# Performance work log

Measured on AMD Instinct MI355X. Metric: run time of the kernel, lower is better.

The kernel has to match this reference:

```python
import jax, jax.numpy as jnp
import numpy as np

B, N, M, D = 64, 512, 1024, 128

def setup_inputs() -> dict:
    key = jax.random.key(0)
    ks = jax.random.split(key, 7)
    s = 1.0 / np.sqrt(D)
    return {
        "h_c": jax.random.normal(ks[0], (B, N, D), dtype=jnp.float32),
        "h_p": jax.random.normal(ks[1], (B, M, D), dtype=jnp.float32),
        "U_w": jax.random.normal(ks[2], (D, D), dtype=jnp.float32) * s,
        "U_b": jax.random.normal(ks[3], (D,), dtype=jnp.float32) * s,
        "V_w": jax.random.normal(ks[4], (D, D), dtype=jnp.float32) * s,
        "V_b": jax.random.normal(ks[5], (D,), dtype=jnp.float32) * s,
        "q": jax.random.normal(ks[6], (D,), dtype=jnp.float32),
    }

def reference(h_c, h_p, U_w, U_b, V_w, V_b, q):
    # ReLU-activated linear projections (torch Linear: x @ W.T + b)
    Uc = jax.nn.relu(jnp.einsum('bnd,ed->bne', h_c, U_w) + U_b)  # (B,N,D)
    Vp = jax.nn.relu(jnp.einsum('bmd,ed->bme', h_p, V_w) + V_b)  # (B,M,D)
    # bilinear attention scores and softmax over protein axis
    attn = jnp.einsum('bnd,bmd->bnm', Uc, Vp)                    # (B,N,M)
    weights = jax.nn.softmax(attn, axis=-1)
    context = jnp.einsum('bnm,bmd->bnd', weights, Vp)            # (B,N,D)
    joint = (Uc + context) * q                                   # (B,N,D)
    return joint.mean(axis=1)                                    # (B,D)
```

## Files before the change

### kernel.cpp

```cpp
#include <hip/hip_runtime.h>
#include <hip/hip_bf16.h>
#include <cstdint>

#define BB 64
#define NN 512
#define MM 1024
#define DD 128

typedef __bf16 bf16x8 __attribute__((ext_vector_type(8)));
typedef float f32x4 __attribute__((ext_vector_type(4)));

static __device__ __forceinline__ unsigned short f2bf(float f) {
    union { float f; unsigned int i; } v; v.f = f;
    unsigned int x = v.i;
    x += 0x7FFFu + ((x >> 16) & 1u);
    return (unsigned short)(x >> 16);
}
static __device__ __forceinline__ unsigned int f2bf2(float a, float b) {
    union { __hip_bfloat162 h; unsigned int u; } c;
    c.h = __float22bfloat162_rn(make_float2(a, b));
    return c.u;
}
static __device__ __forceinline__ void async16(const void* g, void* l) {
    __builtin_amdgcn_global_load_lds(
        (const __attribute__((address_space(1))) void*)g,
        (__attribute__((address_space(3))) void*)l, 16, 0, 0);
}

__global__ __launch_bounds__(256, 4) void proj_v_kernel(
    const float* __restrict__ X,
    const float* __restrict__ Wv,
    const float* __restrict__ bias,
    unsigned short* __restrict__ Y,
    unsigned short* __restrict__ YT)
{
    __shared__ __align__(16) unsigned short Ws[128 * 136];
    unsigned short* Ys = Ws;
    unsigned short* Ts = Ws + 8192;
    const int t = threadIdx.x;
    const int lane = t & 63;
    const int wave = t >> 6;
    const int n16 = lane & 15, q = lane >> 4;
    const long row0 = (long)blockIdx.x * 64;

    float4 xv[8];
    {
        const float* xrow = X + (row0 + wave * 16 + n16) * DD + q * 8;
        #pragma unroll
        for (int kk = 0; kk < 4; ++kk) {
            xv[2 * kk]     = *(const float4*)(xrow + kk * 32);
            xv[2 * kk + 1] = *(const float4*)(xrow + kk * 32 + 4);
        }
    }

    {
        const float4* Wg = (const float4*)Wv;
        #pragma unroll
        for (int i = 0; i < 16; ++i) {
            int idx = i * 256 + t;
            float4 v = Wg[idx];
            int off = idx * 4;
            uint2 u = { f2bf2(v.x, v.y), f2bf2(v.z, v.w) };
            *(uint2*)&Ws[(off >> 7) * 136 + (off & 127)] = u;
        }
    }
    __syncthreads();

    f32x4 acc[8];
    #pragma unroll
    for (int j = 0; j < 8; ++j) acc[j] = {0.f, 0.f, 0.f, 0.f};

    #pragma unroll
    for (int kk = 0; kk < 4; ++kk) {
        float4 x0 = xv[2 * kk], x1 = xv[2 * kk + 1];
        union { bf16x8 v; unsigned int u[4]; } a;
        a.u[0] = f2bf2(x0.x, x0.y); a.u[1] = f2bf2(x0.z, x0.w);
        a.u[2] = f2bf2(x1.x, x1.y); a.u[3] = f2bf2(x1.z, x1.w);
        #pragma unroll
        for (int j = 0; j < 8; ++j) {
            bf16x8 b = *(const bf16x8*)&Ws[(j * 16 + n16) * 136 + q * 8 + kk * 32];
            acc[j] = __builtin_amdgcn_mfma_f32_16x16x32_bf16(a.v, b, acc[j], 0, 0, 0);
        }
    }

    unsigned short yb[8][4];
    #pragma unroll
    for (int j = 0; j < 8; ++j) {
        const float bv = bias[j * 16 + n16];
        float y[4];
        #pragma unroll
        for (int r = 0; r < 4; ++r) {
            float v = acc[j][r] + bv;
            y[r] = v > 0.f ? v : 0.f;
        }
        uint2 u = { f2bf2(y[0], y[1]), f2bf2(y[2], y[3]) };
        *(uint2*)&yb[j][0] = u;
    }
    __syncthreads();

    #pragma unroll
    for (int j = 0; j < 8; ++j) {
        const int e = j * 16 + n16;
        #pragma unroll
        for (int r = 0; r < 4; ++r)
            Ys[(wave * 16 + q * 4 + r) * 128 + e] = yb[j][r];
        *(uint2*)&Ts[e * 72 + wave * 16 + q * 4] = *(uint2*)&yb[j][0];
    }
    __syncthreads();

    {
        uint4* dstY = (uint4*)(Y + row0 * DD);
        const long b = row0 >> 10;
        const long mt = (row0 & 1023) >> 6;
        uint4* dstT = (uint4*)(YT + ((b * 16 + mt) * 128) * 64);
        #pragma unroll
        for (int i = 0; i < 4; ++i) {
            int idx = i * 256 + t;
            dstY[idx] = ((const uint4*)Ys)[idx];
            int e = idx >> 3, m = (idx & 7) * 8;
            dstT[idx] = *(const uint4*)&Ts[e * 72 + m];
        }
    }
}

static __device__ __forceinline__ void bar_lgkm() {
    asm volatile("s_waitcnt lgkmcnt(0)" ::: "memory");
    __builtin_amdgcn_s_barrier();
    __builtin_amdgcn_sched_barrier(0);
}
static __device__ __forceinline__ void bar_vm8() {
    asm volatile("s_waitcnt vmcnt(8) lgkmcnt(0)" ::: "memory");
    __builtin_amdgcn_s_barrier();
    __builtin_amdgcn_sched_barrier(0);
}

static __device__ __forceinline__ void attn_iter(
    int mt, unsigned short* smem, unsigned short* Ps,
    const unsigned short* __restrict__ vpb,
    const unsigned short* __restrict__ vtb,
    int wave, int lane, int n16, int q, int a_off,
    const bf16x8 (&Bg)[4][4],
    bf16x8 (&aC)[4], bf16x8 (&aN)[4],
    f32x4 (&O)[8], float (&lpart)[4])
{
    {
        int nx = mt + 2; if (nx > 15) nx = 15;
        const unsigned short* st = vtb + nx * 8192;
        unsigned short* dst = smem + ((mt + 2) % 3) * 8192 + wave * 2048;
        #pragma unroll
        for (int i = 0; i < 4; ++i) {
            int L = wave * 256 + i * 64 + lane;
            int r = L >> 3, sc = L & 7, c = sc ^ (r & 7);
            async16(st + r * 64 + c * 8, dst + i * 512);
        }
    }
    {
        int nx = mt + 1; if (nx > 15) nx = 15;
        const unsigned short* pa = vpb + nx * 8192 + a_off;
        #pragma unroll
        for (int kk = 0; kk < 4; ++kk)
            aN[kk] = *(const bf16x8*)(pa + kk * 32);
    }

    f32x4 S[4];
    #pragma unroll
    for (int j = 0; j < 4; ++j) S[j] = {0.f, 0.f, 0.f, 0.f};
    __builtin_amdgcn_s_setprio(1);
    #pragma unroll
    for (int kk = 0; kk < 4; ++kk) {
        #pragma unroll
        for (int j = 0; j < 4; ++j)
            S[j] = __builtin_amdgcn_mfma_f32_16x16x32_bf16(aC[kk], Bg[j][kk], S[j], 0, 0, 0);
    }
    __builtin_amdgcn_s_setprio(0);

    #pragma unroll
    for (int j = 0; j < 4; ++j) {
        float p0 = __builtin_exp2f(S[j][0]);
        float p1 = __builtin_exp2f(S[j][1]);
        float p2 = __builtin_exp2f(S[j][2]);
        float p3 = __builtin_exp2f(S[j][3]);
        lpart[j] += (p0 + p1) + (p2 + p3);
        uint2 u = { f2bf2(p0, p1), f2bf2(p2, p3) };
        *(uint2*)&Ps[(j * 16 + n16) * 72 + wave * 16 + q * 4] = u;
    }
    bar_lgkm();

    const unsigned short* VTs = smem + (mt % 3) * 8192;
    __builtin_amdgcn_s_setprio(1);
    #pragma unroll
    for (int kk = 0; kk < 2; ++kk) {
        bf16x8 a = *(const bf16x8*)&Ps[(wave * 16 + n16) * 72 + kk * 32 + q * 8];
        #pragma unroll
        for (int j = 0; j < 8; ++j) {
            bf16x8 bb = *(const bf16x8*)&VTs[(j * 16 + n16) * 64 + ((kk * 4 + q) ^ (n16 & 7)) * 8];
            O[j] = __builtin_amdgcn_mfma_f32_16x16x32_bf16(a, bb, O[j], 0, 0, 0);
        }
    }
    __builtin_amdgcn_s_setprio(0);
    bar_vm8();
}

__global__ __launch_bounds__(256, 2) void attn_kernel(
    const float* __restrict__ hc,
    const float* __restrict__ Wu,
    const float* __restrict__ Ub,
    const unsigned short* __restrict__ Vp,
    const unsigned short* __restrict__ VpT,
    float* __restrict__ part)
{
    __shared__ __align__(16) unsigned short smem[29184];
    unsigned short* Ws  = smem;
    unsigned short* Ucs = smem + 17408;
    unsigned short* Ps  = smem + 24576;

    const int t = threadIdx.x;
    const int lane = t & 63;
    const int wave = t >> 6;
    const int n16 = lane & 15, q = lane >> 4;

    const int id = blockIdx.x;
    const int xcd = id & 7;
    const int slot = id >> 3;
    const int b = xcd * 8 + (slot >> 3);
    const int nt = slot & 7;

    const unsigned short* vpb = Vp + (long)b * MM * DD;
    const unsigned short* vtb = VpT + (long)b * MM * DD;

    const float LOG2E = 1.44269504088896f;

    {
        const float4* Wg = (const float4*)Wu;
        #pragma unroll
        for (int i = 0; i < 16; ++i) {
            int idx = i * 256 + t;
            float4 v = Wg[idx];
            int off = idx * 4;
            uint2 u = { f2bf2(v.x, v.y), f2bf2(v.z, v.w) };
            *(uint2*)&Ws[(off >> 7) * 136 + (off & 127)] = u;
        }
    }
    __syncthreads();

    f32x4 acc[8];
    #pragma unroll
    for (int j = 0; j < 8; ++j) acc[j] = {0.f, 0.f, 0.f, 0.f};
    {
        const float* xrow = hc + ((long)b * NN + nt * 64 + wave * 16 + n16) * DD + q * 8;
        #pragma unroll
        for (int kk = 0; kk < 4; ++kk) {
            float4 x0 = *(const float4*)(xrow + kk * 32);
            float4 x1 = *(const float4*)(xrow + kk * 32 + 4);
            union { bf16x8 v; unsigned int u[4]; } a;
            a.u[0] = f2bf2(x0.x, x0.y); a.u[1] = f2bf2(x0.z, x0.w);
            a.u[2] = f2bf2(x1.x, x1.y); a.u[3] = f2bf2(x1.z, x1.w);
            #pragma unroll
            for (int j = 0; j < 8; ++j) {
                bf16x8 bb = *(const bf16x8*)&Ws[(j * 16 + n16) * 136 + q * 8 + kk * 32];
                acc[j] = __builtin_amdgcn_mfma_f32_16x16x32_bf16(a.v, bb, acc[j], 0, 0, 0);
            }
        }
    }
    float ucred[8];
    #pragma unroll
    for (int j = 0; j < 8; ++j) {
        const float bv = Ub[j * 16 + n16];
        float s = 0.f;
        #pragma unroll
        for (int r = 0; r < 4; ++r) {
            float v = acc[j][r] + bv;
            v = v > 0.f ? v : 0.f;
            s += v;
            Ucs[(wave * 16 + q * 4 + r) * 136 + j * 16 + n16] = f2bf(v * LOG2E);
        }
        ucred[j] = s;
    }
    __syncthreads();

    bf16x8 Bg[4][4];
    #pragma unroll
    for (int j = 0; j < 4; ++j)
        #pragma unroll
        for (int kk = 0; kk < 4; ++kk)
            Bg[j][kk] = *(const bf16x8*)&Ucs[(j * 16 + n16) * 136 + q * 8 + kk * 32];

    const int a_off = (wave * 16 + n16) * 128 + q * 8;
    bf16x8 aA[4], aB[4];
    #pragma unroll
    for (int kk = 0; kk < 4; ++kk)
        aA[kk] = *(const bf16x8*)&vpb[a_off + kk * 32];
    #pragma unroll
    for (int tt = 0; tt < 2; ++tt) {
        const unsigned short* st = vtb + tt * 8192;
        unsigned short* dst = smem + tt * 8192 + wave * 2048;
        #pragma unroll
        for (int i = 0; i < 4; ++i) {
            int L = wave * 256 + i * 64 + lane;
            int r = L >> 3, sc = L & 7, c = sc ^ (r & 7);
            async16(st + r * 64 + c * 8, dst + i * 512);
        }
    }
    asm volatile("s_waitcnt vmcnt(4) lgkmcnt(0)" ::: "memory");
    __builtin_amdgcn_s_barrier();
    __builtin_amdgcn_sched_barrier(0);

    f32x4 O[8];
    #pragma unroll
    for (int j = 0; j < 8; ++j) O[j] = {0.f, 0.f, 0.f, 0.f};
    float lpart[4] = {0.f, 0.f, 0.f, 0.f};

    #pragma unroll 1
    for (int mt = 0; mt < 16; mt += 2) {
        attn_iter(mt,     smem, Ps, vpb, vtb, wave, lane, n16, q, a_off, Bg, aA, aB, O, lpart);
        attn_iter(mt + 1, smem, Ps, vpb, vtb, wave, lane, n16, q, a_off, Bg, aB, aA, O, lpart);
    }

    #pragma unroll
    for (int j = 0; j < 4; ++j) {
        lpart[j] += __shfl_xor(lpart[j], 16);
        lpart[j] += __shfl_xor(lpart[j], 32);
    }
    float* lred = (float*)Ps;
    float* red  = (float*)Ps + 256;
    if (q == 0) {
        #pragma unroll
        for (int j = 0; j < 4; ++j)
            lred[wave * 64 + j * 16 + n16] = lpart[j];
    }
    __syncthreads();

    float inv[4];
    #pragma unroll
    for (int r = 0; r < 4; ++r) {
        int n = wave * 16 + q * 4 + r;
        inv[r] = 1.0f / (lred[n] + lred[64 + n] + lred[128 + n] + lred[192 + n]);
    }

    #pragma unroll
    for (int j = 0; j < 8; ++j) {
        float s = ucred[j]
                + O[j][0] * inv[0] + O[j][1] * inv[1]
                + O[j][2] * inv[2] + O[j][3] * inv[3];
        s += __shfl_xor(s, 16);
        s += __shfl_xor(s, 32);
        if (q == 0)
            red[wave * 128 + j * 16 + n16] = s;
    }
    __syncthreads();
    if (t < 128) {
        float tot = red[t] + red[128 + t] + red[256 + t] + red[384 + t];
        part[(long)(b * 8 + nt) * DD + t] = tot;
    }
}

__global__ __launch_bounds__(256) void finalize_kernel(
    const float* __restrict__ part, const float* __restrict__ qv,
    float* __restrict__ out)
{
    int i = blockIdx.x * 256 + threadIdx.x;
    int b = i >> 7, d = i & 127;
    const float* p = part + (long)b * 8 * DD + d;
    float s = 0.f;
    #pragma unroll
    for (int nt = 0; nt < 8; ++nt) s += p[nt * DD];
    out[i] = s * qv[d] * (1.0f / (float)NN);
}

extern "C" void kernel_launch(void* const* d_in, const int* in_sizes, int n_in,
                              void* d_out, int out_size, void* d_ws, size_t ws_size,
                              hipStream_t stream) {
    const float* h_c = (const float*)d_in[0];
    const float* h_p = (const float*)d_in[1];
    const float* U_w = (const float*)d_in[2];
    const float* U_b = (const float*)d_in[3];
    const float* V_w = (const float*)d_in[4];
    const float* V_b = (const float*)d_in[5];
    const float* qv  = (const float*)d_in[6];
    float* out = (float*)d_out;

    unsigned short* Vp  = (unsigned short*)d_ws;
    unsigned short* VpT = Vp + (size_t)BB * MM * DD;
    float* part = (float*)(VpT + (size_t)BB * MM * DD);

    proj_v_kernel<<<BB * MM / 64, 256, 0, stream>>>(h_p, V_w, V_b, Vp, VpT);
    attn_kernel<<<512, 256, 0, stream>>>(h_c, U_w, U_b, Vp, VpT, part);
    finalize_kernel<<<32, 256, 0, stream>>>(part, qv, out);
}
```

Before: 133.7 us.

## Pre-convert weights once, swizzle LDS layouts, double-buffer V tiles for higher occupancy

Adds a tiny kernel that converts U_w (pre-scaled by log2e) and V_w to bf16 in an XOR-swizzled layout, so every projection block loads ready bf16 weights with async global-to-LDS copies instead of converting fp32 per block. The attention kernel moves from triple- to double-buffered V^T tiles and lets Ps share space with Ucs, shrinking LDS so occupancy can rise from 2 to 3 blocks per CU. Padded LDS rows are replaced by XOR swizzles, and the ucred sum is rescaled by ln2 to undo the folded log2e. This costs an extra launch and leaves less prefetch depth in the V-tile pipeline.

```diff
diff --git a/kernel.cpp b/kernel.cpp
--- a/kernel.cpp
+++ b/kernel.cpp
@@ -27,14 +27,33 @@
         (__attribute__((address_space(3))) void*)l, 16, 0, 0);
 }
 
+__global__ __launch_bounds__(256) void wcvt_kernel(
+    const float* __restrict__ Wu, const float* __restrict__ Wv,
+    unsigned short* __restrict__ out)
+{
+    const float* W = blockIdx.x ? Wv : Wu;
+    unsigned short* o = out + blockIdx.x * 16384;
+    const float s = blockIdx.x ? 1.0f : 1.44269504088896f;
+    #pragma unroll
+    for (int i = 0; i < 8; ++i) {
+        int ch = i * 256 + threadIdx.x;
+        int r = ch >> 4, c = ch & 15;
+        const float4* src = (const float4*)(W + r * 128 + c * 8);
+        float4 a = src[0], b = src[1];
+        uint4 v = { f2bf2(a.x * s, a.y * s), f2bf2(a.z * s, a.w * s),
+                    f2bf2(b.x * s, b.y * s), f2bf2(b.z * s, b.w * s) };
+        *(uint4*)&o[r * 128 + ((c ^ (r & 7)) << 3)] = v;
+    }
+}
+
 __global__ __launch_bounds__(256, 4) void proj_v_kernel(
     const float* __restrict__ X,
-    const float* __restrict__ Wv,
+    const unsigned short* __restrict__ Wvb,
     const float* __restrict__ bias,
     unsigned short* __restrict__ Y,
     unsigned short* __restrict__ YT)
 {
-    __shared__ __align__(16) unsigned short Ws[128 * 136];
+    __shared__ __align__(16) unsigned short Ws[17408];
     unsigned short* Ys = Ws;
     unsigned short* Ts = Ws + 8192;
     const int t = threadIdx.x;
@@ -52,18 +71,9 @@
             xv[2 * kk + 1] = *(const float4*)(xrow + kk * 32 + 4);
         }
     }
-
-    {
-        const float4* Wg = (const float4*)Wv;
-        #pragma unroll
-        for (int i = 0; i < 16; ++i) {
-            int idx = i * 256 + t;
-            float4 v = Wg[idx];
-            int off = idx * 4;
-            uint2 u = { f2bf2(v.x, v.y), f2bf2(v.z, v.w) };
-            *(uint2*)&Ws[(off >> 7) * 136 + (off & 127)] = u;
-        }
-    }
+    #pragma unroll
+    for (int i = 0; i < 8; ++i)
+        async16(Wvb + (wave * 512 + i * 64 + lane) * 8, Ws + wave * 4096 + i * 512);
     __syncthreads();
 
     f32x4 acc[8];
@@ -78,7 +88,8 @@
         a.u[2] = f2bf2(x1.x, x1.y); a.u[3] = f2bf2(x1.z, x1.w);
         #pragma unroll
         for (int j = 0; j < 8; ++j) {
-            bf16x8 b = *(const bf16x8*)&Ws[(j * 16 + n16) * 136 + q * 8 + kk * 32];
+            bf16x8 b = *(const bf16x8*)&Ws[(j * 16 + n16) * 128
+                                           + (((q + 4 * kk) ^ (n16 & 7)) << 3)];
             acc[j] = __builtin_amdgcn_mfma_f32_16x16x32_bf16(a.v, b, acc[j], 0, 0, 0);
         }
     }
@@ -125,11 +136,6 @@
 
 static __device__ __forceinline__ void bar_lgkm() {
     asm volatile("s_waitcnt lgkmcnt(0)" ::: "memory");
-    __builtin_amdgcn_s_barrier();
-    __builtin_amdgcn_sched_barrier(0);
-}
-static __device__ __forceinline__ void bar_vm8() {
-    asm volatile("s_waitcnt vmcnt(8) lgkmcnt(0)" ::: "memory");
     __builtin_amdgcn_s_barrier();
     __builtin_amdgcn_sched_barrier(0);
 }
@@ -143,10 +149,10 @@
     bf16x8 (&aC)[4], bf16x8 (&aN)[4],
     f32x4 (&O)[8], float (&lpart)[4])
 {
-    {
-        int nx = mt + 2; if (nx > 15) nx = 15;
+    const int nx = (mt + 1 > 15) ? 15 : mt + 1;
+    {
         const unsigned short* st = vtb + nx * 8192;
-        unsigned short* dst = smem + ((mt + 2) % 3) * 8192 + wave * 2048;
+        unsigned short* dst = smem + ((mt + 1) & 1) * 8192 + wave * 2048;
         #pragma unroll
         for (int i = 0; i < 4; ++i) {
             int L = wave * 256 + i * 64 + lane;
@@ -154,8 +160,8 @@
             async16(st + r * 64 + c * 8, dst + i * 512);
         }
     }
-    {
-        int nx = mt + 1; if (nx > 15) nx = 15;
+    __builtin_amdgcn_sched_barrier(0);
+    {
         const unsigned short* pa = vpb + nx * 8192 + a_off;
         #pragma unroll
         for (int kk = 0; kk < 4; ++kk)
@@ -186,7 +192,7 @@
     }
     bar_lgkm();
 
-    const unsigned short* VTs = smem + (mt % 3) * 8192;
+    const unsigned short* VTs = smem + (mt & 1) * 8192;
     __builtin_amdgcn_s_setprio(1);
     #pragma unroll
     for (int kk = 0; kk < 2; ++kk) {
@@ -198,21 +204,23 @@
         }
     }
     __builtin_amdgcn_s_setprio(0);
-    bar_vm8();
-}
-
-__global__ __launch_bounds__(256, 2) void attn_kernel(
+    asm volatile("s_waitcnt vmcnt(4) lgkmcnt(0)" ::: "memory");
+    __builtin_amdgcn_s_barrier();
+    __builtin_amdgcn_sched_barrier(0);
+}
+
+__global__ __launch_bounds__(256, 3) void attn_kernel(
     const float* __restrict__ hc,
-    const float* __restrict__ Wu,
+    const unsigned short* __restrict__ Wub,
     const float* __restrict__ Ub,
     const unsigned short* __restrict__ Vp,
     const unsigned short* __restrict__ VpT,
     float* __restrict__ part)
 {
-    __shared__ __align__(16) unsigned short smem[29184];
+    __shared__ __align__(16) unsigned short smem[24576];
     unsigned short* Ws  = smem;
-    unsigned short* Ucs = smem + 17408;
-    unsigned short* Ps  = smem + 24576;
+    unsigned short* Ucs = smem + 16384;
+    unsigned short* Ps  = smem + 16384;
 
     const int t = threadIdx.x;
     const int lane = t & 63;
@@ -229,50 +237,51 @@
     const unsigned short* vtb = VpT + (long)b * MM * DD;
 
     const float LOG2E = 1.44269504088896f;
-
-    {
-        const float4* Wg = (const float4*)Wu;
-        #pragma unroll
-        for (int i = 0; i < 16; ++i) {
-            int idx = i * 256 + t;
-            float4 v = Wg[idx];
-            int off = idx * 4;
-            uint2 u = { f2bf2(v.x, v.y), f2bf2(v.z, v.w) };
-            *(uint2*)&Ws[(off >> 7) * 136 + (off & 127)] = u;
-        }
-    }
+    const float RLN2  = 0.69314718055994531f;
+
+    float4 xv[8];
+    {
+        const float* xrow = hc + ((long)b * NN + nt * 64 + wave * 16 + n16) * DD + q * 8;
+        #pragma unroll
+        for (int kk = 0; kk < 4; ++kk) {
+            xv[2 * kk]     = *(const float4*)(xrow + kk * 32);
+            xv[2 * kk + 1] = *(const float4*)(xrow + kk * 32 + 4);
+        }
+    }
+    #pragma unroll
+    for (int i = 0; i < 8; ++i)
+        async16(Wub + (wave * 512 + i * 64 + lane) * 8, Ws + wave * 4096 + i * 512);
     __syncthreads();
 
     f32x4 acc[8];
     #pragma unroll
     for (int j = 0; j < 8; ++j) acc[j] = {0.f, 0.f, 0.f, 0.f};
-    {
-        const float* xrow = hc + ((long)b * NN + nt * 64 + wave * 16 + n16) * DD + q * 8;
-        #pragma unroll
-        for (int kk = 0; kk < 4; ++kk) {
-            float4 x0 = *(const float4*)(xrow + kk * 32);
-            float4 x1 = *(const float4*)(xrow + kk * 32 + 4);
-            union { bf16x8 v; unsigned int u[4]; } a;
-            a.u[0] = f2bf2(x0.x, x0.y); a.u[1] = f2bf2(x0.z, x0.w);
-            a.u[2] = f2bf2(x1.x, x1.y); a.u[3] = f2bf2(x1.z, x1.w);
-            #pragma unroll
-            for (int j = 0; j < 8; ++j) {
-                bf16x8 bb = *(const bf16x8*)&Ws[(j * 16 + n16) * 136 + q * 8 + kk * 32];
-                acc[j] = __builtin_amdgcn_mfma_f32_16x16x32_bf16(a.v, bb, acc[j], 0, 0, 0);
-            }
+    #pragma unroll
+    for (int kk = 0; kk < 4; ++kk) {
+        float4 x0 = xv[2 * kk], x1 = xv[2 * kk + 1];
+        union { bf16x8 v; unsigned int u[4]; } a;
+        a.u[0] = f2bf2(x0.x, x0.y); a.u[1] = f2bf2(x0.z, x0.w);
+        a.u[2] = f2bf2(x1.x, x1.y); a.u[3] = f2bf2(x1.z, x1.w);
+        #pragma unroll
+        for (int j = 0; j < 8; ++j) {
+            bf16x8 bb = *(const bf16x8*)&Ws[(j * 16 + n16) * 128
+                                            + (((q + 4 * kk) ^ (n16 & 7)) << 3)];
+            acc[j] = __builtin_amdgcn_mfma_f32_16x16x32_bf16(a.v, bb, acc[j], 0, 0, 0);
         }
     }
     float ucred[8];
     #pragma unroll
     for (int j = 0; j < 8; ++j) {
-        const float bv = Ub[j * 16 + n16];
+        const float bv = Ub[j * 16 + n16] * LOG2E;
         float s = 0.f;
         #pragma unroll
         for (int r = 0; r < 4; ++r) {
             float v = acc[j][r] + bv;
             v = v > 0.f ? v : 0.f;
             s += v;
-            Ucs[(wave * 16 + q * 4 + r) * 136 + j * 16 + n16] = f2bf(v * LOG2E);
+            int row = wave * 16 + q * 4 + r;
+            int pc = (2 * j + (n16 >> 3)) ^ (row & 7);
+            Ucs[row * 128 + pc * 8 + (n16 & 7)] = f2bf(v);
         }
         ucred[j] = s;
     }
@@ -283,25 +292,24 @@
     for (int j = 0; j < 4; ++j)
         #pragma unroll
         for (int kk = 0; kk < 4; ++kk)
-            Bg[j][kk] = *(const bf16x8*)&Ucs[(j * 16 + n16) * 136 + q * 8 + kk * 32];
+            Bg[j][kk] = *(const bf16x8*)&Ucs[(j * 16 + n16) * 128
+                                             + (((q + 4 * kk) ^ (n16 & 7)) << 3)];
 
     const int a_off = (wave * 16 + n16) * 128 + q * 8;
     bf16x8 aA[4], aB[4];
     #pragma unroll
     for (int kk = 0; kk < 4; ++kk)
         aA[kk] = *(const bf16x8*)&vpb[a_off + kk * 32];
-    #pragma unroll
-    for (int tt = 0; tt < 2; ++tt) {
-        const unsigned short* st = vtb + tt * 8192;
-        unsigned short* dst = smem + tt * 8192 + wave * 2048;
+    {
+        unsigned short* dst = smem + wave * 2048;
         #pragma unroll
         for (int i = 0; i < 4; ++i) {
             int L = wave * 256 + i * 64 + lane;
             int r = L >> 3, sc = L & 7, c = sc ^ (r & 7);
-            async16(st + r * 64 + c * 8, dst + i * 512);
-        }
-    }
-    asm volatile("s_waitcnt vmcnt(4) lgkmcnt(0)" ::: "memory");
+            async16(vtb + r * 64 + c * 8, dst + i * 512);
+        }
+    }
+    asm volatile("s_waitcnt vmcnt(0) lgkmcnt(0)" ::: "memory");
     __builtin_amdgcn_s_barrier();
     __builtin_amdgcn_sched_barrier(0);
 
@@ -339,7 +347,7 @@
 
     #pragma unroll
     for (int j = 0; j < 8; ++j) {
-        float s = ucred[j]
+        float s = ucred[j] * RLN2
                 + O[j][0] * inv[0] + O[j][1] * inv[1]
                 + O[j][2] * inv[2] + O[j][3] * inv[3];
         s += __shfl_xor(s, 16);
@@ -382,8 +390,10 @@
     unsigned short* Vp  = (unsigned short*)d_ws;
     unsigned short* VpT = Vp + (size_t)BB * MM * DD;
     float* part = (float*)(VpT + (size_t)BB * MM * DD);
-
-    proj_v_kernel<<<BB * MM / 64, 256, 0, stream>>>(h_p, V_w, V_b, Vp, VpT);
-    attn_kernel<<<512, 256, 0, stream>>>(h_c, U_w, U_b, Vp, VpT, part);
+    unsigned short* Wcv = (unsigned short*)(part + (size_t)BB * 8 * DD);
+
+    wcvt_kernel<<<2, 256, 0, stream>>>(U_w, V_w, Wcv);
+    proj_v_kernel<<<BB * MM / 64, 256, 0, stream>>>(h_p, Wcv + 16384, V_b, Vp, VpT);
+    attn_kernel<<<512, 256, 0, stream>>>(h_c, Wcv, U_b, Vp, VpT, part);
     finalize_kernel<<<32, 256, 0, stream>>>(part, qv, out);
 }
```

Result: slower. 174.3 us (+30.4%).
